# Kernel tuning notes

Measured on AMD Instinct MI355X. Metric: run time of the kernel, lower is better.

Reference implementation:

```python
import jax, jax.numpy as jnp
import numpy as np

N = 50000   # nodes
E = 800000  # edges (avg degree 16)
H = 3       # attention heads
D_IN, D_HID, D_OUT = 256, 64, 10


def setup_inputs() -> dict:
    key = jax.random.key(0)
    ks = jax.random.split(key, 8)
    x = jax.random.normal(ks[0], (N, D_IN), dtype=jnp.float32)
    edge_index = jax.random.randint(ks[1], (2, E), 0, N, dtype=jnp.int64)
    W1 = jax.random.normal(ks[2], (H, D_IN, D_HID), dtype=jnp.float32) / np.sqrt(D_IN)
    a_src1 = jax.random.normal(ks[3], (H, D_HID), dtype=jnp.float32) / np.sqrt(D_HID)
    a_dst1 = jax.random.normal(ks[4], (H, D_HID), dtype=jnp.float32) / np.sqrt(D_HID)
    W2 = jax.random.normal(ks[5], (H, D_HID, D_OUT), dtype=jnp.float32) / np.sqrt(D_HID)
    a_src2 = jax.random.normal(ks[6], (H, D_OUT), dtype=jnp.float32) / np.sqrt(D_OUT)
    a_dst2 = jax.random.normal(ks[7], (H, D_OUT), dtype=jnp.float32) / np.sqrt(D_OUT)
    return {"x": x, "edge_index": edge_index, "W1": W1, "a_src1": a_src1,
            "a_dst1": a_dst1, "W2": W2, "a_src2": a_src2, "a_dst2": a_dst2}


def gat_layer(x, src, dst, W, a_s, a_d, n):
    # x: [N, Din]; W: [H, Din, Dout]; returns [N, Dout] (heads averaged)
    z = jnp.einsum('nd,hde->nhe', x, W)                     # [N, H, Dout]
    e_src = jnp.einsum('nhe,he->nh', z, a_s)[src]           # [E, H]
    e_dst = jnp.einsum('nhe,he->nh', z, a_d)[dst]           # [E, H]
    e = jax.nn.leaky_relu(e_src + e_dst, 0.2)               # [E, H]
    # numerically-stable softmax over incoming edges of each dst node
    m = jax.lax.stop_gradient(jax.ops.segment_max(e, dst, num_segments=n))
    ex = jnp.exp(e - m[dst])                                # [E, H]
    denom = jax.ops.segment_sum(ex, dst, num_segments=n)    # [N, H]
    alpha = ex / (denom[dst] + 1e-16)                       # [E, H]
    out = jax.ops.segment_sum(z[src] * alpha[:, :, None], dst, num_segments=n)
    return out.mean(axis=1)                                 # [N, Dout]


def reference(x, edge_index, W1, a_src1, a_dst1, W2, a_src2, a_dst2):
    n = x.shape[0]
    src, dst = edge_index[0], edge_index[1]
    # dropout layers are identity in eval/deterministic mode
    h = gat_layer(x, src, dst, W1, a_src1, a_dst1, n)
    h = jax.nn.elu(h)
    h = gat_layer(h, src, dst, W2, a_src2, a_dst2, n)
    return h, jax.nn.log_softmax(h, axis=1)
```

## Files before the change

kernel.cpp:

```cpp
#include <hip/hip_runtime.h>
#include <math.h>

#define DIN  256
#define DHID 64
#define NH   3
#define DOUT 10
#define CAP  64

typedef __attribute__((ext_vector_type(8))) short bf16x8;
typedef __attribute__((ext_vector_type(4))) float f32x4;

__device__ inline unsigned short f2bf(float f) {
    unsigned u = __builtin_bit_cast(unsigned, f);
    unsigned r = (u + 0x7FFFu + ((u >> 16) & 1u)) >> 16;
    return (unsigned short)r;
}
__device__ inline float bf2f(unsigned short s) {
    unsigned u = ((unsigned)s) << 16;
    return __builtin_bit_cast(float, u);
}
__device__ inline f32x4 cvt4(ushort4 z) {
    f32x4 r;
    r[0] = bf2f(z.x); r[1] = bf2f(z.y); r[2] = bf2f(z.z); r[3] = bf2f(z.w);
    return r;
}


__global__ __launch_bounds__(256) void repack_zero_kernel(const float* __restrict__ W1,
                                                          unsigned short* __restrict__ W1p,
                                                          int* __restrict__ cursor, int N) {
    int bid = blockIdx.x;
    int tid = threadIdx.x;
    if (bid < 192) {
        int idx = bid * 256 + tid;
        int j = idx & 7, l = (idx >> 3) & 63, q = (idx >> 9) & 7, t = idx >> 12;
        int c = t * 16 + (l & 15);
        int k = q * 32 + (l >> 4) * 8 + j;
        int h = c >> 6, jj = c & 63;
        W1p[idx] = f2bf(W1[h * 16384 + k * 64 + jj]);
    } else {
        int i = (bid - 192) * 256 + tid;
        if (i < N) cursor[i] = 0;
    }
}


__global__ __launch_bounds__(256) void gemm1_scatter_kernel(
        const float* __restrict__ x, const bf16x8* __restrict__ W1p,
        const float* __restrict__ a_s, const float* __restrict__ a_d,
        unsigned short* __restrict__ z1bf,
        float* __restrict__ s1, float* __restrict__ d1, int n, int G,
        const int* __restrict__ src, const int* __restrict__ dst,
        int* __restrict__ cursor, int* __restrict__ esrcp, int E) {
    __shared__ unsigned short Xs[64][272];
    int bid = blockIdx.x;
    int tid = threadIdx.x;
    if (bid >= G) {
        int i = (bid - G) * 256 + tid;
        if (i < E) {
            int d = dst[i];
            int s = src[i];
            int pos = atomicAdd(cursor + d, 1);
            if (pos < CAP) esrcp[d * CAP + pos] = s;
        }
        return;
    }
    int w = tid >> 6, lane = tid & 63;
    int m = lane & 15, quad = lane >> 4;
    int n0 = bid * 64;

    for (int i = tid; i < 4096; i += 256) {
        int r = i >> 6, c4 = i & 63;
        int nn = n0 + r;
        float4 a = (nn < n) ? *(const float4*)(x + (size_t)nn * 256 + c4 * 4)
                            : (float4){0.f, 0.f, 0.f, 0.f};
        ushort4 b;
        b.x = f2bf(a.x); b.y = f2bf(a.y); b.z = f2bf(a.z); b.w = f2bf(a.w);
        *(ushort4*)(&Xs[r][c4 * 4]) = b;
    }
    __syncthreads();

    int rloc = w * 16 + m;
    f32x4 acc[12];
    #pragma unroll
    for (int t = 0; t < 12; ++t) acc[t] = (f32x4){0.f, 0.f, 0.f, 0.f};
    #pragma unroll
    for (int q = 0; q < 8; ++q) {
        bf16x8 af = *(const bf16x8*)(&Xs[rloc][q * 32 + quad * 8]);
        #pragma unroll
        for (int t = 0; t < 12; ++t) {
            bf16x8 bfr = W1p[(t * 8 + q) * 64 + lane];
            acc[t] = __builtin_amdgcn_mfma_f32_16x16x32_bf16(af, bfr, acc[t], 0, 0, 0);
        }
    }
    __syncthreads();

    float as_r[12], ad_r[12];
    #pragma unroll
    for (int t = 0; t < 12; ++t) { as_r[t] = a_s[t * 16 + m]; ad_r[t] = a_d[t * 16 + m]; }

    #pragma unroll
    for (int reg = 0; reg < 4; ++reg) {
        int row_loc = w * 16 + quad * 4 + reg;
        int row_out = n0 + row_loc;
        bool ok = row_out < n;
        float ps[3] = {0.f, 0.f, 0.f}, pd[3] = {0.f, 0.f, 0.f};
        #pragma unroll
        for (int t = 0; t < 12; ++t) {
            float v = acc[t][reg];
            Xs[row_loc][t * 16 + m] = f2bf(v);
            ps[t >> 2] += v * as_r[t];
            pd[t >> 2] += v * ad_r[t];
        }
        #pragma unroll
        for (int h = 0; h < 3; ++h) {
            float s = ps[h], d = pd[h];
            #pragma unroll
            for (int msk = 1; msk < 16; msk <<= 1) {
                s += __shfl_xor(s, msk, 16);
                d += __shfl_xor(d, msk, 16);
            }
            if (ok && m == 0) { s1[row_out * 4 + h] = s; d1[row_out * 4 + h] = d; }
        }
    }
    __syncthreads();

    for (int i = tid; i < 3072; i += 256) {
        int r = i / 48, c4 = i % 48;
        int nn = n0 + r;
        if (nn < n)
            *(ushort4*)(z1bf + (size_t)nn * 192 + c4 * 4) = *(const ushort4*)(&Xs[r][c4 * 4]);
    }
}


__global__ __launch_bounds__(256) void agg1_kernel(const int* __restrict__ cnts,
                                                   const int* __restrict__ esrcp,
                                                   const float* __restrict__ s1,
                                                   const float* __restrict__ d1,
                                                   const unsigned short* __restrict__ z1bf,
                                                   float* __restrict__ h1, int n) {
    __shared__ float wlds[4][196];
    int tid = threadIdx.x;
    int lane = tid & 63, wave = tid >> 6;
    int v = blockIdx.x * 4 + wave;
    if (v >= n) return;
    int cnt = cnts[v]; if (cnt > CAP) cnt = CAP;
    int m16 = lane & 15;
    int grp = lane >> 4;
    int head = grp > 2 ? 2 : grp;
    bool rowact = lane < 48;
    float dv0 = d1[v * 4], dv1 = d1[v * 4 + 1], dv2 = d1[v * 4 + 2];
    float* wl = wlds[wave];

    int u_l = 0; float w0 = 0.f, w1 = 0.f, w2 = 0.f;
    if (lane < cnt) {
        u_l = esrcp[v * CAP + lane];
        float4 sv = *(const float4*)(s1 + (size_t)u_l * 4);
        float e0 = sv.x + dv0; e0 = e0 > 0.f ? e0 : 0.2f * e0;
        float e1 = sv.y + dv1; e1 = e1 > 0.f ? e1 : 0.2f * e1;
        float e2 = sv.z + dv2; e2 = e2 > 0.f ? e2 : 0.2f * e2;
        w0 = __expf(e0); w1 = __expf(e1); w2 = __expf(e2);
    }
    wl[lane] = w0; wl[65 + lane] = w1; wl[130 + lane] = w2;
    float4 wv = *(const float4*)(&wl[head * 65 + m16 * 4]);
    float denp = wv.x + wv.y + wv.z + wv.w;
    #pragma unroll
    for (int msk = 1; msk < 16; msk <<= 1) denp += __shfl_xor(denp, msk, 16);

    f32x4 acc = (f32x4){0.f, 0.f, 0.f, 0.f};
    if (rowact) {
        int rnd = (cnt + 3) & ~3;
        const int wb = head * 65;
        for (int j = 0; j < rnd; j += 4) {
            int u0 = __builtin_amdgcn_readlane(u_l, j);
            int u1 = __builtin_amdgcn_readlane(u_l, j + 1);
            int u2 = __builtin_amdgcn_readlane(u_l, j + 2);
            int u3 = __builtin_amdgcn_readlane(u_l, j + 3);
            float wa = wl[wb + j], wb2 = wl[wb + j + 1];
            float wc = wl[wb + j + 2], wd = wl[wb + j + 3];
            ushort4 za = *(const ushort4*)(z1bf + (size_t)u0 * 192 + lane * 4);
            ushort4 zb = *(const ushort4*)(z1bf + (size_t)u1 * 192 + lane * 4);
            ushort4 zc = *(const ushort4*)(z1bf + (size_t)u2 * 192 + lane * 4);
            ushort4 zd = *(const ushort4*)(z1bf + (size_t)u3 * 192 + lane * 4);
            acc += cvt4(za) * wa;
            acc += cvt4(zb) * wb2;
            acc += cvt4(zc) * wc;
            acc += cvt4(zd) * wd;
        }
    }
    float invd = (1.f / 3.f) / (denp + 1e-16f);
    float acc0 = rowact ? acc[0] * invd : 0.f;
    float acc1 = rowact ? acc[1] * invd : 0.f;
    float acc2 = rowact ? acc[2] * invd : 0.f;
    float acc3 = rowact ? acc[3] * invd : 0.f;
    acc0 += __shfl_down(acc0, 32, 64); acc0 += __shfl_down(acc0, 16, 64);
    acc1 += __shfl_down(acc1, 32, 64); acc1 += __shfl_down(acc1, 16, 64);
    acc2 += __shfl_down(acc2, 32, 64); acc2 += __shfl_down(acc2, 16, 64);
    acc3 += __shfl_down(acc3, 32, 64); acc3 += __shfl_down(acc3, 16, 64);
    if (lane < 16) {
        float4 o;
        o.x = acc0 > 0.f ? acc0 : __expf(acc0) - 1.f;
        o.y = acc1 > 0.f ? acc1 : __expf(acc1) - 1.f;
        o.z = acc2 > 0.f ? acc2 : __expf(acc2) - 1.f;
        o.w = acc3 > 0.f ? acc3 : __expf(acc3) - 1.f;
        *(float4*)(h1 + (size_t)v * 64 + lane * 4) = o;
    }
}


__global__ __launch_bounds__(256) void gemm2_kernel(const float* __restrict__ h1,
                                                    const float* __restrict__ W2,
                                                    const float* __restrict__ as2,
                                                    const float* __restrict__ ad2,
                                                    unsigned short* __restrict__ z2bf,
                                                    float* __restrict__ s2,
                                                    float* __restrict__ d2, int n) {
    __shared__ float Xs[32][65];
    __shared__ float Ws[64][32];
    __shared__ float Zs[32][33];
    int tid = threadIdx.x;
    int tx = tid % 32, ty = tid / 32;
    int n0 = blockIdx.x * 32;
    for (int idx = tid; idx < 64 * 32; idx += 256) {
        int kk = idx >> 5, c = idx & 31;
        float wv = 0.f;
        if (c < 30) {
            int h = c / 10, j = c % 10;
            wv = W2[(h * 64 + kk) * 10 + j];
        }
        Ws[kk][c] = wv;
    }
    for (int idx = tid; idx < 32 * 64; idx += 256) {
        int r = idx >> 6, kk = idx & 63;
        int nn = n0 + r;
        Xs[r][kk] = (nn < n) ? h1[(size_t)nn * 64 + kk] : 0.f;
    }
    __syncthreads();
    float acc[4] = {0.f, 0.f, 0.f, 0.f};
    #pragma unroll 8
    for (int kk = 0; kk < 64; ++kk) {
        float w = Ws[kk][tx];
        #pragma unroll
        for (int p = 0; p < 4; ++p) acc[p] += Xs[ty + 8 * p][kk] * w;
    }
    #pragma unroll
    for (int p = 0; p < 4; ++p) {
        int rloc = ty + 8 * p;
        int nn = n0 + rloc;
        float val = tx < 30 ? acc[p] : 0.f;
        Zs[rloc][tx] = val;
        if (nn < n) z2bf[(size_t)nn * 32 + tx] = f2bf(val);
    }
    __syncthreads();
    if (tid < 96) {
        int rloc = tid / 3, h = tid % 3;
        int nn = n0 + rloc;
        if (nn < n) {
            float ss = 0.f, dd = 0.f;
            #pragma unroll
            for (int j = 0; j < 10; ++j) {
                float z = Zs[rloc][h * 10 + j];
                ss += z * as2[h * 10 + j];
                dd += z * ad2[h * 10 + j];
            }
            s2[nn * 4 + h] = ss;
            d2[nn * 4 + h] = dd;
        }
    }
}


__global__ __launch_bounds__(256) void agg2_kernel(const int* __restrict__ cnts,
                                                   const int* __restrict__ esrcp,
                                                   const float* __restrict__ s2,
                                                   const float* __restrict__ d2,
                                                   const unsigned short* __restrict__ z2bf,
                                                   float* __restrict__ out, int n) {
    __shared__ float wlds[4][196];
    __shared__ float dlds[4][4];
    int tid = threadIdx.x;
    int lane = tid & 63, wave = tid >> 6;
    int v = blockIdx.x * 4 + wave;
    if (v >= n) return;
    int cnt = cnts[v]; if (cnt > CAP) cnt = CAP;
    int c2 = lane & 15;
    int quad = lane >> 4;
    int headc = c2 < 5 ? 0 : (c2 < 10 ? 1 : 2);
    int headg = quad > 2 ? 2 : quad;
    float dv0 = d2[v * 4], dv1 = d2[v * 4 + 1], dv2 = d2[v * 4 + 2];
    float* wl = wlds[wave];

    int u_l = 0; float w0 = 0.f, w1 = 0.f, w2 = 0.f;
    if (lane < cnt) {
        u_l = esrcp[v * CAP + lane];
        float4 sv = *(const float4*)(s2 + (size_t)u_l * 4);
        float e0 = sv.x + dv0; e0 = e0 > 0.f ? e0 : 0.2f * e0;
        float e1 = sv.y + dv1; e1 = e1 > 0.f ? e1 : 0.2f * e1;
        float e2 = sv.z + dv2; e2 = e2 > 0.f ? e2 : 0.2f * e2;
        w0 = __expf(e0); w1 = __expf(e1); w2 = __expf(e2);
    }
    wl[lane] = w0; wl[65 + lane] = w1; wl[130 + lane] = w2;
    float4 wv = *(const float4*)(&wl[headg * 65 + c2 * 4]);
    float denp = wv.x + wv.y + wv.z + wv.w;
    #pragma unroll
    for (int msk = 1; msk < 16; msk <<= 1) denp += __shfl_xor(denp, msk, 16);
    if (c2 == 0 && quad < 3) dlds[wave][quad] = denp;

    float ax = 0.f, ay = 0.f;
    int rnd = (cnt + 3) & ~3;
    const int wb = headc * 65;
    for (int j = 0; j < rnd; j += 4) {
        int u = __shfl(u_l, j + quad, 64);
        float w = wl[wb + j + quad];
        ushort2 z = *(const ushort2*)(z2bf + (size_t)u * 32 + c2 * 2);
        ax += w * bf2f(z.x);
        ay += w * bf2f(z.y);
    }
    float den = dlds[wave][headc];
    ax += __shfl_down(ax, 32, 64); ax += __shfl_down(ax, 16, 64);
    ay += __shfl_down(ay, 32, 64); ay += __shfl_down(ay, 16, 64);
    float inv = 1.f / (den + 1e-16f);
    float rx = ax * inv, ry = ay * inv;
    float rx5  = __shfl(rx, lane + 5, 64);
    float rx10 = __shfl(rx, lane + 10, 64);
    float ry5  = __shfl(ry, lane + 5, 64);
    float ry10 = __shfl(ry, lane + 10, 64);
    float rrx = (rx + rx5 + rx10) * (1.f / 3.f);
    float rry = (ry + ry5 + ry10) * (1.f / 3.f);
    bool act = lane < 5;
    float mx = act ? fmaxf(rrx, rry) : -1e30f;
    #pragma unroll
    for (int msk = 1; msk < 8; msk <<= 1) mx = fmaxf(mx, __shfl_xor(mx, msk, 8));
    float e = act ? (__expf(rrx - mx) + __expf(rry - mx)) : 0.f;
    #pragma unroll
    for (int msk = 1; msk < 8; msk <<= 1) e += __shfl_xor(e, msk, 8);
    float lg = __logf(e);
    if (act) {
        float2 o1; o1.x = rrx; o1.y = rry;
        float2 o2; o2.x = rrx - mx - lg; o2.y = rry - mx - lg;
        *(float2*)(out + (size_t)v * DOUT + c2 * 2) = o1;
        *(float2*)(out + (size_t)n * DOUT + (size_t)v * DOUT + c2 * 2) = o2;
    }
}


extern "C" void kernel_launch(void* const* d_in, const int* in_sizes, int n_in,
                              void* d_out, int out_size, void* d_ws, size_t ws_size,
                              hipStream_t stream) {
    const float* x   = (const float*)d_in[0];
    const int*   ei  = (const int*)d_in[1];
    const float* W1  = (const float*)d_in[2];
    const float* as1 = (const float*)d_in[3];
    const float* ad1 = (const float*)d_in[4];
    const float* W2  = (const float*)d_in[5];
    const float* as2 = (const float*)d_in[6];
    const float* ad2 = (const float*)d_in[7];
    float* out = (float*)d_out;

    const int N = in_sizes[0] / DIN;
    const int E = in_sizes[1] / 2;
    const int* src = ei;
    const int* dst = ei + E;

    char* p = (char*)d_ws;
    auto alloc = [&](size_t bytes) -> void* {
        void* r = (void*)p;
        p += (bytes + 255) & ~(size_t)255;
        return r;
    };
    int* cursor  = (int*)alloc((size_t)N * 4);
    int* esrcp   = (int*)alloc((size_t)N * CAP * 4);
    unsigned short* W1p  = (unsigned short*)alloc((size_t)49152 * 2);
    unsigned short* z1bf = (unsigned short*)alloc((size_t)N * 192 * 2);
    float* s1    = (float*)alloc((size_t)N * 4 * 4);
    float* d1    = (float*)alloc((size_t)N * 4 * 4);
    float* h1    = (float*)alloc((size_t)N * 64 * 4);
    unsigned short* z2bf = (unsigned short*)alloc((size_t)N * 32 * 2);
    float* s2    = (float*)alloc((size_t)N * 4 * 4);
    float* d2    = (float*)alloc((size_t)N * 4 * 4);
    (void)alloc(512);

    repack_zero_kernel<<<192 + (N + 255) / 256, 256, 0, stream>>>(W1, W1p, cursor, N);

    int G = (N + 63) / 64;
    int S = (E + 255) / 256;
    gemm1_scatter_kernel<<<G + S, 256, 0, stream>>>(
        x, (const bf16x8*)W1p, as1, ad1, z1bf, s1, d1, N, G,
        src, dst, cursor, esrcp, E);

    agg1_kernel<<<(N + 3) / 4, 256, 0, stream>>>(cursor, esrcp, s1, d1, z1bf, h1, N);
    gemm2_kernel<<<(N + 31) / 32, 256, 0, stream>>>(h1, W2, as2, ad2, z2bf, s2, d2, N);
    agg2_kernel<<<(N + 3) / 4, 256, 0, stream>>>(cursor, esrcp, s2, d2, z2bf, out, N);
}
```

Before: 275.5 us.

## Split fused gemm1+scatter into separate kernels and shrink gemm1 tile to 32 rows

Undoes the fusion of the edge scatter with the first-layer GEMM, launching the scatter as its own kernel ahead of the GEMM. The GEMM block now covers 32 rows with 128 threads (2 waves) instead of 64 rows with 256 threads, which halves LDS per block and doubles the block count. The aim is better occupancy and load balance for the GEMM. The cost is one extra kernel launch and losing the overlap between scatter atomics and GEMM work.

```diff
diff --git a/kernel.cpp b/kernel.cpp
--- a/kernel.cpp
+++ b/kernel.cpp
@@ -45,31 +45,34 @@
 }
 
 
-__global__ __launch_bounds__(256) void gemm1_scatter_kernel(
-        const float* __restrict__ x, const bf16x8* __restrict__ W1p,
-        const float* __restrict__ a_s, const float* __restrict__ a_d,
-        unsigned short* __restrict__ z1bf,
-        float* __restrict__ s1, float* __restrict__ d1, int n, int G,
-        const int* __restrict__ src, const int* __restrict__ dst,
-        int* __restrict__ cursor, int* __restrict__ esrcp, int E) {
-    __shared__ unsigned short Xs[64][272];
-    int bid = blockIdx.x;
-    int tid = threadIdx.x;
-    if (bid >= G) {
-        int i = (bid - G) * 256 + tid;
-        if (i < E) {
-            int d = dst[i];
-            int s = src[i];
-            int pos = atomicAdd(cursor + d, 1);
-            if (pos < CAP) esrcp[d * CAP + pos] = s;
-        }
-        return;
-    }
+__global__ __launch_bounds__(256) void scatter_kernel(const int* __restrict__ src,
+                                                      const int* __restrict__ dst,
+                                                      int* __restrict__ cursor,
+                                                      int* __restrict__ esrcp, int E) {
+    int i = blockIdx.x * 256 + threadIdx.x;
+    if (i < E) {
+        int d = dst[i];
+        int s = src[i];
+        int pos = atomicAdd(cursor + d, 1);
+        if (pos < CAP) esrcp[d * CAP + pos] = s;
+    }
+}
+
+
+__global__ __launch_bounds__(128) void gemm1_mfma_kernel(const float* __restrict__ x,
+                                                         const bf16x8* __restrict__ W1p,
+                                                         const float* __restrict__ a_s,
+                                                         const float* __restrict__ a_d,
+                                                         unsigned short* __restrict__ z1bf,
+                                                         float* __restrict__ s1,
+                                                         float* __restrict__ d1, int n) {
+    __shared__ unsigned short Xs[32][272];
+    int tid = threadIdx.x;
     int w = tid >> 6, lane = tid & 63;
     int m = lane & 15, quad = lane >> 4;
-    int n0 = bid * 64;
-
-    for (int i = tid; i < 4096; i += 256) {
+    int n0 = blockIdx.x * 32;
+
+    for (int i = tid; i < 2048; i += 128) {
         int r = i >> 6, c4 = i & 63;
         int nn = n0 + r;
         float4 a = (nn < n) ? *(const float4*)(x + (size_t)nn * 256 + c4 * 4)
@@ -125,7 +128,7 @@
     }
     __syncthreads();
 
-    for (int i = tid; i < 3072; i += 256) {
+    for (int i = tid; i < 1536; i += 128) {
         int r = i / 48, c4 = i % 48;
         int nn = n0 + r;
         if (nn < n)
@@ -382,13 +385,10 @@
     (void)alloc(512);
 
     repack_zero_kernel<<<192 + (N + 255) / 256, 256, 0, stream>>>(W1, W1p, cursor, N);
-
-    int G = (N + 63) / 64;
-    int S = (E + 255) / 256;
-    gemm1_scatter_kernel<<<G + S, 256, 0, stream>>>(
-        x, (const bf16x8*)W1p, as1, ad1, z1bf, s1, d1, N, G,
-        src, dst, cursor, esrcp, E);
-
+    scatter_kernel<<<(E + 255) / 256, 256, 0, stream>>>(src, dst, cursor, esrcp, E);
+
+    gemm1_mfma_kernel<<<(N + 31) / 32, 128, 0, stream>>>(x, (const bf16x8*)W1p, as1, ad1,
+                                                         z1bf, s1, d1, N);
     agg1_kernel<<<(N + 3) / 4, 256, 0, stream>>>(cursor, esrcp, s1, d1, z1bf, h1, N);
     gemm2_kernel<<<(N + 31) / 32, 256, 0, stream>>>(h1, W2, as2, ad2, z2bf, s2, d2, N);
     agg2_kernel<<<(N + 3) / 4, 256, 0, stream>>>(cursor, esrcp, s2, d2, z2bf, out, N);
```

Result: faster. 257.6 us (-6.5%).
